# Kernel optimization log

Measured on AMD Instinct MI355X. Metric: run time of the kernel, lower is better.

Reference implementation:

```python
import jax, jax.numpy as jnp
import numpy as np

NUM_EXPERTS = 8
TOP_K = 2


def setup_inputs() -> dict:
    key = jax.random.key(0)
    k1, k2, k3, k4, k5 = jax.random.split(key, 5)
    B, S, H, I, E = 2, 2048, 1024, 3584, NUM_EXPERTS
    scale_h = 1.0 / np.sqrt(H)
    scale_i = 1.0 / np.sqrt(I)
    return {
        "hidden_states": jax.random.normal(k1, (B, S, H), dtype=jnp.float32),
        "gate_w": jax.random.normal(k2, (H, E), dtype=jnp.float32) * scale_h,
        "w1": jax.random.normal(k3, (E, H, I), dtype=jnp.float32) * scale_h,
        "w3": jax.random.normal(k4, (E, H, I), dtype=jnp.float32) * scale_h,
        "w2": jax.random.normal(k5, (E, I, H), dtype=jnp.float32) * scale_i,
    }


def reference(hidden_states, gate_w, w1, w3, w2):
    # Router: [B,S,H] @ [H,E] -> [B,S,E]
    router_logits = jnp.einsum("bsh,he->bse", hidden_states, gate_w).astype(jnp.float32)
    routing_weights, selected_experts = jax.lax.top_k(router_logits, k=TOP_K)
    routing_weights = jax.nn.softmax(routing_weights, axis=-1)  # [B,S,TOP_K]

    final_hidden_state = jnp.zeros_like(hidden_states)
    # Dense loop over all experts (faithful to the original mask-multiply-accumulate)
    for index in range(NUM_EXPERTS):
        h1 = jax.nn.silu(jnp.einsum("bsh,hi->bsi", hidden_states, w1[index]))
        h3 = jnp.einsum("bsh,hi->bsi", hidden_states, w3[index])
        expert_out = jnp.einsum("bsi,ih->bsh", h1 * h3, w2[index])
        # Per-token routing weight for this expert (0 if not selected)
        weight = jnp.sum(
            jnp.where(selected_experts == index, routing_weights, 0.0), axis=-1
        )[:, :, None]  # [B,S,1]
        final_hidden_state = final_hidden_state + weight * expert_out
    return final_hidden_state, router_logits
```

## Files before the change

### kernel.cpp

```cpp
#include <hip/hip_runtime.h>


typedef __bf16 v8bf __attribute__((ext_vector_type(8)));
typedef float  v4f  __attribute__((ext_vector_type(4)));

constexpr int kT = 4096;
constexpr int kH = 1024;
constexpr int kI = 3584;
constexpr int kE = 8;

constexpr size_t SZ_W    = (size_t)kE * kI * kH * 2;
constexpr size_t OFF_W1T = 0;
constexpr size_t OFF_W3T = OFF_W1T + SZ_W;
constexpr size_t OFF_W2T = OFF_W3T + SZ_W;
constexpr size_t OFF_XG  = OFF_W2T + SZ_W;
constexpr size_t OFF_ACT = OFF_XG  + (size_t)2*kT*kH*2;
constexpr size_t OFF_BUF = OFF_ACT + (size_t)2*kT*kI*2;
constexpr size_t OFF_CNT = OFF_BUF + (size_t)2*kT*kH*4;
constexpr size_t OFF_OFS = OFF_CNT + 128;
constexpr size_t OFF_LST = OFF_OFS + 128;
constexpr size_t OFF_TW  = OFF_LST + (size_t)kE*kT*4;
constexpr size_t OFF_TR  = OFF_TW  + (size_t)kT*2*4;

__device__ __forceinline__ void async16(void* lds, const void* g) {
    __builtin_amdgcn_global_load_lds(
        (const __attribute__((address_space(1))) unsigned int*)g,
        (__attribute__((address_space(3))) unsigned int*)lds,
        16, 0, 0);
}

__global__ void zero_counts_kernel(int* __restrict__ counts) {
    if (threadIdx.x < kE) counts[threadIdx.x] = 0;
}

__global__ void prefix_kernel(const int* __restrict__ counts, int* __restrict__ offsets) {
    if (threadIdx.x == 0) {
        int o = 0;
        for (int e = 0; e < kE; e++) { offsets[e] = o; o += counts[e]; }
    }
}

__global__ void router_kernel(const float* __restrict__ x, const float* __restrict__ gw,
                              float* __restrict__ logits_out, float* __restrict__ tw,
                              int* __restrict__ counts, int* __restrict__ list) {
    const int wave = threadIdx.x >> 6;
    const int lane = threadIdx.x & 63;
    const int t = blockIdx.x * 4 + wave;
    const float* xr = x + (size_t)t * kH;

    double acc[kE];
#pragma unroll
    for (int e = 0; e < kE; e++) acc[e] = 0.0;

    for (int j = 0; j < kH / 64; j++) {
        const int h = j * 64 + lane;
        const float xv = xr[h];
        const float* g = gw + (size_t)h * kE;
#pragma unroll
        for (int e = 0; e < kE; e++) acc[e] += (double)xv * (double)g[e];
    }
#pragma unroll
    for (int e = 0; e < kE; e++) {
#pragma unroll
        for (int o = 32; o > 0; o >>= 1) acc[e] += __shfl_xor(acc[e], o, 64);
    }

    if (lane == 0) {
        float lg[kE];
#pragma unroll
        for (int e = 0; e < kE; e++) lg[e] = (float)acc[e];
#pragma unroll
        for (int e = 0; e < kE; e++) logits_out[(size_t)t * kE + e] = lg[e];

        int e0 = 0; float l0 = lg[0];
        for (int e = 1; e < kE; e++) if (lg[e] > l0) { l0 = lg[e]; e0 = e; }
        int e1 = -1; float l1 = -3.4e38f;
        for (int e = 0; e < kE; e++) if (e != e0 && lg[e] > l1) { l1 = lg[e]; e1 = e; }

        const float ex = __expf(l1 - l0);
        const float w0 = 1.0f / (1.0f + ex);
        const float w1 = ex / (1.0f + ex);

        int s0 = atomicAdd(&counts[e0], 1);
        list[e0 * kT + s0] = t * 2 + 0;
        tw[t * 2 + 0] = w0;
        int s1 = atomicAdd(&counts[e1], 1);
        list[e1 * kT + s1] = t * 2 + 1;
        tw[t * 2 + 1] = w1;
    }
}

__global__ void gather_kernel(const float* __restrict__ x, const int* __restrict__ list,
                              const int* __restrict__ counts, const int* __restrict__ offsets,
                              __bf16* __restrict__ xg, int* __restrict__ trow) {
    const int g = blockIdx.x;
    int e = 0;
    while (e < kE - 1 && g >= offsets[e] + counts[e]) e++;
    const int s = g - offsets[e];
    const int entry = list[e * kT + s];
    const int t = entry >> 1;
    if (threadIdx.x == 0) trow[entry] = g;
    const int i = threadIdx.x * 4;
    const float4 v = *(const float4*)&x[(size_t)t * kH + i];
    __bf16 pk[4] = {(__bf16)v.x, (__bf16)v.y, (__bf16)v.z, (__bf16)v.w};
    *(ushort4*)&xg[(size_t)g * kH + i] = *(const ushort4*)pk;
}

__global__ void transpose_cvt_kernel(const float* __restrict__ srcA, const float* __restrict__ srcB,
                                     __bf16* __restrict__ dstA, __bf16* __restrict__ dstB,
                                     int R, int C, int nz) {
    __shared__ float tile[64][65];
    const int z = blockIdx.z;
    const float* s;
    __bf16* d;
    if (z < nz) { s = srcA + (size_t)z * R * C;        d = dstA + (size_t)z * R * C; }
    else        { s = srcB + (size_t)(z - nz) * R * C; d = dstB + (size_t)(z - nz) * R * C; }
    const int r0 = blockIdx.y * 64, c0 = blockIdx.x * 64;
    const int tr = threadIdx.x >> 4;
    const int tc = (threadIdx.x & 15) * 4;
#pragma unroll
    for (int i = 0; i < 4; i++) {
        const float4 v = *(const float4*)&s[(size_t)(r0 + tr + i * 16) * C + (c0 + tc)];
        tile[tr + i * 16][tc + 0] = v.x;
        tile[tr + i * 16][tc + 1] = v.y;
        tile[tr + i * 16][tc + 2] = v.z;
        tile[tr + i * 16][tc + 3] = v.w;
    }
    __syncthreads();
#pragma unroll
    for (int i = 0; i < 4; i++) {
        const int oc = tr + i * 16;
        __bf16 pk[4] = {(__bf16)tile[tc + 0][oc], (__bf16)tile[tc + 1][oc],
                        (__bf16)tile[tc + 2][oc], (__bf16)tile[tc + 3][oc]};
        *(ushort4*)&d[(size_t)(c0 + oc) * R + r0 + tc] = *(const ushort4*)pk;
    }
}

__global__ __launch_bounds__(256, 2) void gemm1_kernel(
    const __bf16* __restrict__ xg, const __bf16* __restrict__ w1t,
    const __bf16* __restrict__ w3t, __bf16* __restrict__ act,
    const int* __restrict__ counts, const int* __restrict__ offsets) {
    const int e = blockIdx.z;
    const int cnt = counts[e];
    const int m0 = blockIdx.y * 128;
    if (m0 >= cnt) return;
    const int n0 = blockIdx.x * 128;
    const int off = offsets[e];

    __shared__ __bf16 As[128 * 32], B1s[128 * 32], B3s[128 * 32];

    const int tid = threadIdx.x;
    const int lane = tid & 63, wave = tid >> 6;
    const int wm = (wave >> 1) * 64, wn = (wave & 1) * 64;
    const int lrow = lane & 15, quad = lane >> 4;

    const int scol = (((tid & 3) ^ ((tid >> 2) & 3) ^ ((tid >> 4) & 3))) * 8;
    const __bf16* abase[2];
    const __bf16* b1base[2];
    const __bf16* b3base[2];
    const __bf16* w1b = w1t + (size_t)e * kI * kH + (size_t)n0 * kH;
    const __bf16* w3b = w3t + (size_t)e * kI * kH + (size_t)n0 * kH;
#pragma unroll
    for (int p = 0; p < 2; p++) {
        const int r = p * 64 + (tid >> 2);
        const int gr = min(m0 + r, cnt - 1);
        abase[p]  = xg + (size_t)(off + gr) * kH + scol;
        b1base[p] = w1b + (size_t)r * kH + scol;
        b3base[p] = w3b + (size_t)r * kH + scol;
    }

    const int sw = (lane & 3) ^ ((lane >> 2) & 3);
    const int fragoff = lrow * 32 + ((quad ^ sw) * 8);

    v4f acc1[4][4], acc3[4][4];
#pragma unroll
    for (int i = 0; i < 4; i++)
#pragma unroll
        for (int j = 0; j < 4; j++) { acc1[i][j] = (v4f)0.0f; acc3[i][j] = (v4f)0.0f; }

    for (int kt = 0; kt < kH / 32; kt++) {
        const int k0 = kt * 32;
#pragma unroll
        for (int p = 0; p < 2; p++) {
            const int soff = p * 2048 + tid * 8;
            async16(&As[soff],  abase[p]  + k0);
            async16(&B1s[soff], b1base[p] + k0);
            async16(&B3s[soff], b3base[p] + k0);
        }
        __syncthreads();

        v8bf a[4];
#pragma unroll
        for (int fm = 0; fm < 4; fm++)
            a[fm] = *(const v8bf*)&As[(wm + fm * 16) * 32 + fragoff];
#pragma unroll
        for (int fn = 0; fn < 4; fn++) {
            const v8bf b1 = *(const v8bf*)&B1s[(wn + fn * 16) * 32 + fragoff];
            const v8bf b3 = *(const v8bf*)&B3s[(wn + fn * 16) * 32 + fragoff];
#pragma unroll
            for (int fm = 0; fm < 4; fm++) {
                acc1[fm][fn] = __builtin_amdgcn_mfma_f32_16x16x32_bf16(a[fm], b1, acc1[fm][fn], 0, 0, 0);
                acc3[fm][fn] = __builtin_amdgcn_mfma_f32_16x16x32_bf16(a[fm], b3, acc3[fm][fn], 0, 0, 0);
            }
        }
        __syncthreads();
    }

#pragma unroll
    for (int fm = 0; fm < 4; fm++) {
#pragma unroll
        for (int fn = 0; fn < 4; fn++) {
            const v4f c1 = acc1[fm][fn], c3 = acc3[fm][fn];
            const int col = n0 + wn + fn * 16 + lrow;
#pragma unroll
            for (int r = 0; r < 4; r++) {
                const int gm = m0 + wm + fm * 16 + quad * 4 + r;
                if (gm < cnt) {
                    const float h1 = c1[r], h3 = c3[r];
                    const float v = h1 / (1.0f + __expf(-h1)) * h3;
                    act[(size_t)(off + gm) * kI + col] = (__bf16)v;
                }
            }
        }
    }
}

__global__ __launch_bounds__(256, 2) void gemm2_kernel(
    const __bf16* __restrict__ act, const __bf16* __restrict__ w2t,
    float* __restrict__ buf,
    const int* __restrict__ counts, const int* __restrict__ offsets) {
    const int e = blockIdx.z;
    const int cnt = counts[e];
    const int m0 = blockIdx.y * 128;
    if (m0 >= cnt) return;
    const int n0 = blockIdx.x * 128;
    const int off = offsets[e];

    __shared__ __bf16 As[128 * 32], Bs[128 * 32];

    const int tid = threadIdx.x;
    const int lane = tid & 63, wave = tid >> 6;
    const int wm = (wave >> 1) * 64, wn = (wave & 1) * 64;
    const int lrow = lane & 15, quad = lane >> 4;

    const int scol = (((tid & 3) ^ ((tid >> 2) & 3) ^ ((tid >> 4) & 3))) * 8;
    const __bf16* abase[2];
    const __bf16* bbase[2];
    const __bf16* w2b = w2t + (size_t)e * kH * kI + (size_t)n0 * kI;
#pragma unroll
    for (int p = 0; p < 2; p++) {
        const int r = p * 64 + (tid >> 2);
        const int gr = min(m0 + r, cnt - 1);
        abase[p] = act + (size_t)(off + gr) * kI + scol;
        bbase[p] = w2b + (size_t)r * kI + scol;
    }

    const int sw = (lane & 3) ^ ((lane >> 2) & 3);
    const int fragoff = lrow * 32 + ((quad ^ sw) * 8);

    v4f acc[4][4];
#pragma unroll
    for (int i = 0; i < 4; i++)
#pragma unroll
        for (int j = 0; j < 4; j++) acc[i][j] = (v4f)0.0f;

    for (int kt = 0; kt < kI / 32; kt++) {
        const int k0 = kt * 32;
#pragma unroll
        for (int p = 0; p < 2; p++) {
            const int soff = p * 2048 + tid * 8;
            async16(&As[soff], abase[p] + k0);
            async16(&Bs[soff], bbase[p] + k0);
        }
        __syncthreads();

        v8bf a[4];
#pragma unroll
        for (int fm = 0; fm < 4; fm++)
            a[fm] = *(const v8bf*)&As[(wm + fm * 16) * 32 + fragoff];
#pragma unroll
        for (int fn = 0; fn < 4; fn++) {
            const v8bf b = *(const v8bf*)&Bs[(wn + fn * 16) * 32 + fragoff];
#pragma unroll
            for (int fm = 0; fm < 4; fm++)
                acc[fm][fn] = __builtin_amdgcn_mfma_f32_16x16x32_bf16(a[fm], b, acc[fm][fn], 0, 0, 0);
        }
        __syncthreads();
    }

#pragma unroll
    for (int fm = 0; fm < 4; fm++) {
#pragma unroll
        for (int fn = 0; fn < 4; fn++) {
            const v4f c = acc[fm][fn];
            const int col = n0 + wn + fn * 16 + lrow;
#pragma unroll
            for (int r = 0; r < 4; r++) {
                const int gm = m0 + wm + fm * 16 + quad * 4 + r;
                if (gm < cnt) buf[(size_t)(off + gm) * kH + col] = c[r];
            }
        }
    }
}

__global__ void combine_kernel(const float* __restrict__ buf, const int* __restrict__ trow,
                               const float* __restrict__ tw, float* __restrict__ out) {
    const int t = blockIdx.x;
    const int r0 = trow[2 * t], r1 = trow[2 * t + 1];
    const float w0 = tw[2 * t], w1 = tw[2 * t + 1];
    const int i = threadIdx.x * 4;
    const float4 a = *(const float4*)&buf[(size_t)r0 * kH + i];
    const float4 b = *(const float4*)&buf[(size_t)r1 * kH + i];
    float4 o;
    o.x = w0 * a.x + w1 * b.x;
    o.y = w0 * a.y + w1 * b.y;
    o.z = w0 * a.z + w1 * b.z;
    o.w = w0 * a.w + w1 * b.w;
    *(float4*)&out[(size_t)t * kH + i] = o;
}

extern "C" void kernel_launch(void* const* d_in, const int* in_sizes, int n_in,
                              void* d_out, int out_size, void* d_ws, size_t ws_size,
                              hipStream_t stream) {
    const float* x  = (const float*)d_in[0];
    const float* gw = (const float*)d_in[1];
    const float* w1 = (const float*)d_in[2];
    const float* w3 = (const float*)d_in[3];
    const float* w2 = (const float*)d_in[4];
    float* out = (float*)d_out;
    float* logits_out = out + (size_t)kT * kH;

    char* ws = (char*)d_ws;
    __bf16* w1t   = (__bf16*)(ws + OFF_W1T);
    __bf16* w3t   = (__bf16*)(ws + OFF_W3T);
    __bf16* w2t   = (__bf16*)(ws + OFF_W2T);
    __bf16* xg    = (__bf16*)(ws + OFF_XG);
    __bf16* act   = (__bf16*)(ws + OFF_ACT);
    float*  buf   = (float*) (ws + OFF_BUF);
    int*    cnt   = (int*)   (ws + OFF_CNT);
    int*    ofs   = (int*)   (ws + OFF_OFS);
    int*    list  = (int*)   (ws + OFF_LST);
    float*  tw    = (float*) (ws + OFF_TW);
    int*    trow  = (int*)   (ws + OFF_TR);

    zero_counts_kernel<<<1, 64, 0, stream>>>(cnt);

    transpose_cvt_kernel<<<dim3(kI / 64, kH / 64, 2 * kE), 256, 0, stream>>>(
        w1, w3, w1t, w3t, kH, kI, kE);
    transpose_cvt_kernel<<<dim3(kH / 64, kI / 64, kE), 256, 0, stream>>>(
        w2, w2, w2t, w2t, kI, kH, kE);

    router_kernel<<<kT / 4, 256, 0, stream>>>(x, gw, logits_out, tw, cnt, list);
    prefix_kernel<<<1, 1, 0, stream>>>(cnt, ofs);
    gather_kernel<<<2 * kT, 256, 0, stream>>>(x, list, cnt, ofs, xg, trow);

    gemm1_kernel<<<dim3(kI / 128, kT / 128, kE), 256, 0, stream>>>(xg, w1t, w3t, act, cnt, ofs);
    gemm2_kernel<<<dim3(kH / 128, kT / 128, kE), 256, 0, stream>>>(act, w2t, buf, cnt, ofs);

    combine_kernel<<<kT, 256, 0, stream>>>(buf, trow, tw, out);
}
```

Baseline: 788.0 us.

## Switch expert GEMMs to 32x32x16 MFMA and merge weight transpose launches

Both expert GEMM kernels now use the 32x32x16 bf16 MFMA with 2x2 fragments per wave instead of 4x4 16x16x32 fragments. The LDS swizzle and fragment offsets change to match the new operand layout. The three weight transpose/convert passes are merged into one launch with a flattened tile index. The fp32 output buffer is aliased onto the w1t region, which gemm1 no longer needs once it finishes, to shrink the workspace. Larger MFMA tiles cut LDS fragment loads per FLOP, but the aliasing depends on strict stream ordering between the kernels.

Result: slower. 816.4 us (+3.6%).

```diff
diff --git a/kernel.cpp b/kernel.cpp
--- a/kernel.cpp
+++ b/kernel.cpp
@@ -1,8 +1,8 @@
 #include <hip/hip_runtime.h>
 
 
-typedef __bf16 v8bf __attribute__((ext_vector_type(8)));
-typedef float  v4f  __attribute__((ext_vector_type(4)));
+typedef __bf16 v8bf  __attribute__((ext_vector_type(8)));
+typedef float  v16f  __attribute__((ext_vector_type(16)));
 
 constexpr int kT = 4096;
 constexpr int kH = 1024;
@@ -15,8 +15,8 @@
 constexpr size_t OFF_W2T = OFF_W3T + SZ_W;
 constexpr size_t OFF_XG  = OFF_W2T + SZ_W;
 constexpr size_t OFF_ACT = OFF_XG  + (size_t)2*kT*kH*2;
-constexpr size_t OFF_BUF = OFF_ACT + (size_t)2*kT*kI*2;
-constexpr size_t OFF_CNT = OFF_BUF + (size_t)2*kT*kH*4;
+constexpr size_t OFF_BUF = OFF_W1T;
+constexpr size_t OFF_CNT = OFF_ACT + (size_t)2*kT*kI*2;
 constexpr size_t OFF_OFS = OFF_CNT + 128;
 constexpr size_t OFF_LST = OFF_OFS + 128;
 constexpr size_t OFF_TW  = OFF_LST + (size_t)kE*kT*4;
@@ -106,16 +106,19 @@
     *(ushort4*)&xg[(size_t)g * kH + i] = *(const ushort4*)pk;
 }
 
-__global__ void transpose_cvt_kernel(const float* __restrict__ srcA, const float* __restrict__ srcB,
-                                     __bf16* __restrict__ dstA, __bf16* __restrict__ dstB,
-                                     int R, int C, int nz) {
+__global__ void transpose_cvt_all_kernel(const float* __restrict__ w1, const float* __restrict__ w3,
+                                         const float* __restrict__ w2,
+                                         __bf16* __restrict__ w1t, __bf16* __restrict__ w3t,
+                                         __bf16* __restrict__ w2t) {
     __shared__ float tile[64][65];
     const int z = blockIdx.z;
-    const float* s;
-    __bf16* d;
-    if (z < nz) { s = srcA + (size_t)z * R * C;        d = dstA + (size_t)z * R * C; }
-    else        { s = srcB + (size_t)(z - nz) * R * C; d = dstB + (size_t)(z - nz) * R * C; }
-    const int r0 = blockIdx.y * 64, c0 = blockIdx.x * 64;
+    const float* s; __bf16* d; int R, C;
+    if (z < 8)       { s = w1 + (size_t)z * kH * kI;        d = w1t + (size_t)z * kH * kI;        R = kH; C = kI; }
+    else if (z < 16) { s = w3 + (size_t)(z - 8) * kH * kI;  d = w3t + (size_t)(z - 8) * kH * kI;  R = kH; C = kI; }
+    else             { s = w2 + (size_t)(z - 16) * kI * kH; d = w2t + (size_t)(z - 16) * kI * kH; R = kI; C = kH; }
+    const int ntx = C / 64;
+    const int tx = blockIdx.x % ntx, ty = blockIdx.x / ntx;
+    const int r0 = ty * 64, c0 = tx * 64;
     const int tr = threadIdx.x >> 4;
     const int tc = (threadIdx.x & 15) * 4;
 #pragma unroll
@@ -152,9 +155,10 @@
     const int tid = threadIdx.x;
     const int lane = tid & 63, wave = tid >> 6;
     const int wm = (wave >> 1) * 64, wn = (wave & 1) * 64;
-    const int lrow = lane & 15, quad = lane >> 4;
-
-    const int scol = (((tid & 3) ^ ((tid >> 2) & 3) ^ ((tid >> 4) & 3))) * 8;
+    const int l31 = lane & 31;
+    const int half = lane >> 5;
+
+    const int scol = ((tid & 3) ^ ((tid >> 2) & 3)) * 8;
     const __bf16* abase[2];
     const __bf16* b1base[2];
     const __bf16* b3base[2];
@@ -169,14 +173,14 @@
         b3base[p] = w3b + (size_t)r * kH + scol;
     }
 
-    const int sw = (lane & 3) ^ ((lane >> 2) & 3);
-    const int fragoff = lrow * 32 + ((quad ^ sw) * 8);
-
-    v4f acc1[4][4], acc3[4][4];
-#pragma unroll
-    for (int i = 0; i < 4; i++)
-#pragma unroll
-        for (int j = 0; j < 4; j++) { acc1[i][j] = (v4f)0.0f; acc3[i][j] = (v4f)0.0f; }
+    const int ph0 = (half ^ (lane & 3)) * 8;
+    const int ph1 = ((half ^ 2) ^ (lane & 3)) * 8;
+
+    v16f acc1[2][2], acc3[2][2];
+#pragma unroll
+    for (int i = 0; i < 2; i++)
+#pragma unroll
+        for (int j = 0; j < 2; j++) { acc1[i][j] = (v16f)0.0f; acc3[i][j] = (v16f)0.0f; }
 
     for (int kt = 0; kt < kH / 32; kt++) {
         const int k0 = kt * 32;
@@ -189,34 +193,39 @@
         }
         __syncthreads();
 
-        v8bf a[4];
-#pragma unroll
-        for (int fm = 0; fm < 4; fm++)
-            a[fm] = *(const v8bf*)&As[(wm + fm * 16) * 32 + fragoff];
-#pragma unroll
-        for (int fn = 0; fn < 4; fn++) {
-            const v8bf b1 = *(const v8bf*)&B1s[(wn + fn * 16) * 32 + fragoff];
-            const v8bf b3 = *(const v8bf*)&B3s[(wn + fn * 16) * 32 + fragoff];
-#pragma unroll
-            for (int fm = 0; fm < 4; fm++) {
-                acc1[fm][fn] = __builtin_amdgcn_mfma_f32_16x16x32_bf16(a[fm], b1, acc1[fm][fn], 0, 0, 0);
-                acc3[fm][fn] = __builtin_amdgcn_mfma_f32_16x16x32_bf16(a[fm], b3, acc3[fm][fn], 0, 0, 0);
+#pragma unroll
+        for (int ks = 0; ks < 2; ks++) {
+            const int ph = ks ? ph1 : ph0;
+            v8bf a[2], b1[2], b3[2];
+#pragma unroll
+            for (int f = 0; f < 2; f++) {
+                a[f]  = *(const v8bf*)&As [(wm + f * 32 + l31) * 32 + ph];
+                b1[f] = *(const v8bf*)&B1s[(wn + f * 32 + l31) * 32 + ph];
+                b3[f] = *(const v8bf*)&B3s[(wn + f * 32 + l31) * 32 + ph];
             }
+#pragma unroll
+            for (int fn = 0; fn < 2; fn++)
+#pragma unroll
+                for (int fm = 0; fm < 2; fm++) {
+                    acc1[fm][fn] = __builtin_amdgcn_mfma_f32_32x32x16_bf16(a[fm], b1[fn], acc1[fm][fn], 0, 0, 0);
+                    acc3[fm][fn] = __builtin_amdgcn_mfma_f32_32x32x16_bf16(a[fm], b3[fn], acc3[fm][fn], 0, 0, 0);
+                }
         }
         __syncthreads();
     }
 
 #pragma unroll
-    for (int fm = 0; fm < 4; fm++) {
-#pragma unroll
-        for (int fn = 0; fn < 4; fn++) {
-            const v4f c1 = acc1[fm][fn], c3 = acc3[fm][fn];
-            const int col = n0 + wn + fn * 16 + lrow;
-#pragma unroll
-            for (int r = 0; r < 4; r++) {
-                const int gm = m0 + wm + fm * 16 + quad * 4 + r;
+    for (int fm = 0; fm < 2; fm++) {
+#pragma unroll
+        for (int fn = 0; fn < 2; fn++) {
+            const v16f c1 = acc1[fm][fn], c3 = acc3[fm][fn];
+            const int col = n0 + wn + fn * 32 + l31;
+#pragma unroll
+            for (int reg = 0; reg < 16; reg++) {
+                const int rloc = (reg & 3) + 8 * (reg >> 2) + 4 * half;
+                const int gm = m0 + wm + fm * 32 + rloc;
                 if (gm < cnt) {
-                    const float h1 = c1[r], h3 = c3[r];
+                    const float h1 = c1[reg], h3 = c3[reg];
                     const float v = h1 / (1.0f + __expf(-h1)) * h3;
                     act[(size_t)(off + gm) * kI + col] = (__bf16)v;
                 }
@@ -241,9 +250,10 @@
     const int tid = threadIdx.x;
     const int lane = tid & 63, wave = tid >> 6;
     const int wm = (wave >> 1) * 64, wn = (wave & 1) * 64;
-    const int lrow = lane & 15, quad = lane >> 4;
-
-    const int scol = (((tid & 3) ^ ((tid >> 2) & 3) ^ ((tid >> 4) & 3))) * 8;
+    const int l31 = lane & 31;
+    const int half = lane >> 5;
+
+    const int scol = ((tid & 3) ^ ((tid >> 2) & 3)) * 8;
     const __bf16* abase[2];
     const __bf16* bbase[2];
     const __bf16* w2b = w2t + (size_t)e * kH * kI + (size_t)n0 * kI;
@@ -255,14 +265,14 @@
         bbase[p] = w2b + (size_t)r * kI + scol;
     }
 
-    const int sw = (lane & 3) ^ ((lane >> 2) & 3);
-    const int fragoff = lrow * 32 + ((quad ^ sw) * 8);
-
-    v4f acc[4][4];
-#pragma unroll
-    for (int i = 0; i < 4; i++)
-#pragma unroll
-        for (int j = 0; j < 4; j++) acc[i][j] = (v4f)0.0f;
+    const int ph0 = (half ^ (lane & 3)) * 8;
+    const int ph1 = ((half ^ 2) ^ (lane & 3)) * 8;
+
+    v16f acc[2][2];
+#pragma unroll
+    for (int i = 0; i < 2; i++)
+#pragma unroll
+        for (int j = 0; j < 2; j++) acc[i][j] = (v16f)0.0f;
 
     for (int kt = 0; kt < kI / 32; kt++) {
         const int k0 = kt * 32;
@@ -274,30 +284,35 @@
         }
         __syncthreads();
 
-        v8bf a[4];
-#pragma unroll
-        for (int fm = 0; fm < 4; fm++)
-            a[fm] = *(const v8bf*)&As[(wm + fm * 16) * 32 + fragoff];
-#pragma unroll
-        for (int fn = 0; fn < 4; fn++) {
-            const v8bf b = *(const v8bf*)&Bs[(wn + fn * 16) * 32 + fragoff];
-#pragma unroll
-            for (int fm = 0; fm < 4; fm++)
-                acc[fm][fn] = __builtin_amdgcn_mfma_f32_16x16x32_bf16(a[fm], b, acc[fm][fn], 0, 0, 0);
+#pragma unroll
+        for (int ks = 0; ks < 2; ks++) {
+            const int ph = ks ? ph1 : ph0;
+            v8bf a[2], b[2];
+#pragma unroll
+            for (int f = 0; f < 2; f++) {
+                a[f] = *(const v8bf*)&As[(wm + f * 32 + l31) * 32 + ph];
+                b[f] = *(const v8bf*)&Bs[(wn + f * 32 + l31) * 32 + ph];
+            }
+#pragma unroll
+            for (int fn = 0; fn < 2; fn++)
+#pragma unroll
+                for (int fm = 0; fm < 2; fm++)
+                    acc[fm][fn] = __builtin_amdgcn_mfma_f32_32x32x16_bf16(a[fm], b[fn], acc[fm][fn], 0, 0, 0);
         }
         __syncthreads();
     }
 
 #pragma unroll
-    for (int fm = 0; fm < 4; fm++) {
-#pragma unroll
-        for (int fn = 0; fn < 4; fn++) {
-            const v4f c = acc[fm][fn];
-            const int col = n0 + wn + fn * 16 + lrow;
-#pragma unroll
-            for (int r = 0; r < 4; r++) {
-                const int gm = m0 + wm + fm * 16 + quad * 4 + r;
-                if (gm < cnt) buf[(size_t)(off + gm) * kH + col] = c[r];
+    for (int fm = 0; fm < 2; fm++) {
+#pragma unroll
+        for (int fn = 0; fn < 2; fn++) {
+            const v16f c = acc[fm][fn];
+            const int col = n0 + wn + fn * 32 + l31;
+#pragma unroll
+            for (int reg = 0; reg < 16; reg++) {
+                const int rloc = (reg & 3) + 8 * (reg >> 2) + 4 * half;
+                const int gm = m0 + wm + fm * 32 + rloc;
+                if (gm < cnt) buf[(size_t)(off + gm) * kH + col] = c[reg];
             }
         }
     }
@@ -345,10 +360,7 @@
 
     zero_counts_kernel<<<1, 64, 0, stream>>>(cnt);
 
-    transpose_cvt_kernel<<<dim3(kI / 64, kH / 64, 2 * kE), 256, 0, stream>>>(
-        w1, w3, w1t, w3t, kH, kI, kE);
-    transpose_cvt_kernel<<<dim3(kH / 64, kI / 64, kE), 256, 0, stream>>>(
-        w2, w2, w2t, w2t, kI, kH, kE);
+    transpose_cvt_all_kernel<<<dim3(896, 1, 24), 256, 0, stream>>>(w1, w3, w2, w1t, w3t, w2t);
 
     router_kernel<<<kT / 4, 256, 0, stream>>>(x, gw, logits_out, tw, cnt, list);
     prefix_kernel<<<1, 1, 0, stream>>>(cnt, ofs);
```
